# Kernel tuning notes

Measured on AMD Instinct MI355X. Metric: run time of the kernel, lower is better.

## Reference

```python
import jax, jax.numpy as jnp
import numpy as np

N_NODES = 100000
N_EDGES = 1600000
NUM_FEATURES = 128


def setup_inputs() -> dict:
    key = jax.random.key(0)
    ks = jax.random.split(key, 10)
    x = jax.random.normal(ks[0], (N_NODES, NUM_FEATURES), dtype=jnp.float32)
    edge_index = jax.random.randint(ks[1], (2, N_EDGES), 0, N_NODES, dtype=jnp.int64)
    # conv1 MLP: Linear(num_features,128) -> ReLU -> Linear(128,128)
    s1 = 1.0 / np.sqrt(NUM_FEATURES)
    W1 = jax.random.uniform(ks[2], (NUM_FEATURES, 128), jnp.float32, -s1, s1)
    b1 = jax.random.uniform(ks[3], (128,), jnp.float32, -s1, s1)
    s2 = 1.0 / np.sqrt(128)
    W2 = jax.random.uniform(ks[4], (128, 128), jnp.float32, -s2, s2)
    b2 = jax.random.uniform(ks[5], (128,), jnp.float32, -s2, s2)
    # conv2 MLP: Linear(128,64) -> ReLU -> Linear(64,64)
    W3 = jax.random.uniform(ks[6], (128, 64), jnp.float32, -s2, s2)
    b3 = jax.random.uniform(ks[7], (64,), jnp.float32, -s2, s2)
    s3 = 1.0 / np.sqrt(64)
    W4 = jax.random.uniform(ks[8], (64, 64), jnp.float32, -s3, s3)
    b4 = jax.random.uniform(ks[9], (64,), jnp.float32, -s3, s3)
    return {"x": x, "edge_index": edge_index, "W1": W1, "b1": b1,
            "W2": W2, "b2": b2, "W3": W3, "b3": b3, "W4": W4, "b4": b4}


def _gin_conv(x, src, dst, Wa, ba, Wb, bb):
    # GINConv with eps=0: out = MLP(x + sum_{j->i} x_j)
    agg = jax.ops.segment_sum(x[src], dst, num_segments=N_NODES)
    h = x + agg
    h = jax.nn.relu(h @ Wa + ba)
    return h @ Wb + bb


def reference(x, edge_index, W1, b1, W2, b2, W3, b3, W4, b4):
    src, dst = edge_index[0], edge_index[1]
    h = jax.nn.relu(_gin_conv(x, src, dst, W1, b1, W2, b2))
    h = jax.nn.relu(_gin_conv(h, src, dst, W3, b3, W4, b4))
    return h
```

## Files before the change

kernel.cpp:

```cpp
#include <hip/hip_runtime.h>
#include <hip/hip_bf16.h>

#define NODES 100000
#define EDGES 1600000
#define NBINS ((NODES + 127) >> 7)
#define BINCAP 2560
#define PB_BLOCKS 256
#define PB_CHUNK ((EDGES + PB_BLOCKS - 1) / PB_BLOCKS)
#define CAST_BLOCKS 12500
#define WPREP_BLOCKS 176

typedef __bf16 bf16x8 __attribute__((ext_vector_type(8)));
typedef float f32x4 __attribute__((ext_vector_type(4)));

__device__ __forceinline__ unsigned short f2b(float f) {
  __hip_bfloat16 h = __float2bfloat16(f);
  return __builtin_bit_cast(unsigned short, h);
}
__device__ __forceinline__ float b_lo(unsigned u) { return __uint_as_float(u << 16); }
__device__ __forceinline__ float b_hi(unsigned u) { return __uint_as_float(u & 0xffff0000u); }

__global__ __launch_bounds__(256) void prep_count(
    const float4* __restrict__ x4, ushort4* __restrict__ xh4,
    const float* __restrict__ W1, const float* __restrict__ W2,
    const float* __restrict__ W3, const float* __restrict__ W4,
    unsigned short* __restrict__ Wt1, unsigned short* __restrict__ Wt2,
    unsigned short* __restrict__ Wt3, unsigned short* __restrict__ Wt4,
    int* __restrict__ cnt) {
  const int b = blockIdx.x;
  if (b < CAST_BLOCKS) {
    int i = b * 256 + threadIdx.x;
    float4 v = x4[i];
    ushort4 o;
    o.x = f2b(v.x); o.y = f2b(v.y); o.z = f2b(v.z); o.w = f2b(v.w);
    xh4[i] = o;
    return;
  }
  if (b < CAST_BLOCKS + WPREP_BLOCKS) {
    int i = (b - CAST_BLOCKS) * 256 + threadIdx.x;
    if (i < 16384) {
      int n = i >> 7, k = i & 127;
      Wt1[i] = f2b(W1[k * 128 + n]);
    } else if (i < 32768) {
      int j = i - 16384; int n = j >> 7, k = j & 127;
      Wt2[j] = f2b(W2[k * 128 + n]);
    } else if (i < 40960) {
      int j = i - 32768; int n = j >> 7, k = j & 127;
      Wt3[j] = f2b(W3[k * 64 + n]);
    } else if (i < 45056) {
      int j = i - 40960; int n = j >> 6, k = j & 63;
      Wt4[j] = f2b(W4[k * 64 + n]);
    }
    return;
  }
  for (int i = threadIdx.x; i < NBINS; i += 256) cnt[i] = 0;
}

__global__ __launch_bounds__(256) void bin_scatter(const int* __restrict__ src,
                                                   const int* __restrict__ dst,
                                                   int* __restrict__ cnt,
                                                   unsigned* __restrict__ coarse) {
  __shared__ int base[NBINS];
  __shared__ int h[NBINS];
  const int beg = blockIdx.x * PB_CHUNK;
  const int end = min(beg + PB_CHUNK, EDGES);
  for (int i = threadIdx.x; i < NBINS; i += 256) h[i] = 0;
  __syncthreads();
  for (int e = beg + threadIdx.x; e < end; e += 256)
    atomicAdd(&h[dst[e] >> 7], 1);
  __syncthreads();
  for (int i = threadIdx.x; i < NBINS; i += 256) {
    int c = h[i];
    if (c > 0) base[i] = atomicAdd(&cnt[i], c);
    h[i] = 0;
  }
  __syncthreads();
  for (int e = beg + threadIdx.x; e < end; e += 256) {
    int d = dst[e];
    int b = d >> 7;
    int pos = base[b] + atomicAdd(&h[b], 1);
    coarse[(size_t)b * BINCAP + pos] = (unsigned)src[e] | ((unsigned)(d & 127) << 17);
  }
}

__global__ __launch_bounds__(256) void bin_fine(const unsigned* __restrict__ coarse,
                                                const int* __restrict__ cnt,
                                                int2* __restrict__ rowpairs,
                                                int* __restrict__ bucket) {
  __shared__ unsigned ent[BINCAP];
  __shared__ unsigned obuf[BINCAP];
  __shared__ int deg[128];
  __shared__ int pre[128];
  const int b = blockIdx.x;
  const int t = threadIdx.x;
  const int s0 = b * BINCAP;
  const int nE = cnt[b];
  const int binBase = b << 7;

  if (t < 128) deg[t] = 0;
  __syncthreads();
  for (int i = t; i < nE; i += 256) {
    unsigned e = coarse[s0 + i];
    ent[i] = e;
    atomicAdd(&deg[e >> 17], 1);
  }
  __syncthreads();
  int v = 0;
  if (t < 128) {
    v = deg[t];
    pre[t] = v;
  }
  __syncthreads();
  for (int off = 1; off < 128; off <<= 1) {
    int u = (t >= off && t < 128) ? pre[t - off] : 0;
    __syncthreads();
    if (t < 128) pre[t] += u;
    __syncthreads();
  }
  if (t < 128) {
    int inc = pre[t];
    int ex = inc - v;
    if (binBase + t < NODES) rowpairs[binBase + t] = make_int2(s0 + ex, s0 + inc);
    deg[t] = ex;
  }
  __syncthreads();
  for (int i = t; i < nE; i += 256) {
    unsigned e = ent[i];
    int pos = atomicAdd(&deg[e >> 17], 1);
    obuf[pos] = e & 0x1FFFFu;
  }
  __syncthreads();
  for (int i = t; i < nE; i += 256) bucket[s0 + i] = (int)obuf[i];
}

#define ACC8(r, m)                                                            \
  a[0] = fmaf(b_lo(r.x), m, a[0]); a[1] = fmaf(b_hi(r.x), m, a[1]);           \
  a[2] = fmaf(b_lo(r.y), m, a[2]); a[3] = fmaf(b_hi(r.y), m, a[3]);           \
  a[4] = fmaf(b_lo(r.z), m, a[4]); a[5] = fmaf(b_hi(r.z), m, a[5]);           \
  a[6] = fmaf(b_lo(r.w), m, a[6]); a[7] = fmaf(b_hi(r.w), m, a[7]);

template <int K, int N1, int N2, bool OUT_F32>
__global__ __launch_bounds__(256, 6) void gin_layer(
    const uint4* __restrict__ xq, const int2* __restrict__ rowpairs,
    const int* __restrict__ bucket,
    const unsigned short* __restrict__ Wa, const float* __restrict__ ba,
    const unsigned short* __restrict__ Wb, const float* __restrict__ bb,
    void* __restrict__ Cout, int M) {
  constexpr int LDA = K + 8;
  constexpr int NT1 = N1 / 16, KB1 = K / 32;
  constexpr int NT2 = N2 / 16, KB2 = N1 / 32;
  __shared__ unsigned short S[64 * LDA];

  const int tid = threadIdx.x;
  const int wave = tid >> 6;
  const int lane = tid & 63;
  const int g = lane >> 4;
  const int fl = lane & 15;
  const int rowBase = blockIdx.x * 64;

  for (int p = 0; p < 4; p++) {
    const int rloc = wave * 16 + p * 4 + g;
    const int n = rowBase + rloc;
    float a[8] = {0.f, 0.f, 0.f, 0.f, 0.f, 0.f, 0.f, 0.f};
    if (n < M) {
      uint4 v = xq[(size_t)n * 16 + fl];
      a[0] = b_lo(v.x); a[1] = b_hi(v.x);
      a[2] = b_lo(v.y); a[3] = b_hi(v.y);
      a[4] = b_lo(v.z); a[5] = b_hi(v.z);
      a[6] = b_lo(v.w); a[7] = b_hi(v.w);
      const int2 se = rowpairs[n];
      const int beg = se.x, end = se.y;
      for (int j = beg; j < end; j += 8) {
        int i1 = min(j + 1, end - 1), i2 = min(j + 2, end - 1),
            i3 = min(j + 3, end - 1), i4 = min(j + 4, end - 1),
            i5 = min(j + 5, end - 1), i6 = min(j + 6, end - 1),
            i7 = min(j + 7, end - 1);
        int s0 = bucket[j],  s1 = bucket[i1], s2 = bucket[i2], s3 = bucket[i3];
        int s4 = bucket[i4], s5 = bucket[i5], s6 = bucket[i6], s7 = bucket[i7];
        uint4 r0 = xq[(size_t)s0 * 16 + fl];
        uint4 r1 = xq[(size_t)s1 * 16 + fl];
        uint4 r2 = xq[(size_t)s2 * 16 + fl];
        uint4 r3 = xq[(size_t)s3 * 16 + fl];
        uint4 r4 = xq[(size_t)s4 * 16 + fl];
        uint4 r5 = xq[(size_t)s5 * 16 + fl];
        uint4 r6 = xq[(size_t)s6 * 16 + fl];
        uint4 r7 = xq[(size_t)s7 * 16 + fl];
        float m1 = (j + 1 < end) ? 1.f : 0.f;
        float m2 = (j + 2 < end) ? 1.f : 0.f;
        float m3 = (j + 3 < end) ? 1.f : 0.f;
        float m4 = (j + 4 < end) ? 1.f : 0.f;
        float m5 = (j + 5 < end) ? 1.f : 0.f;
        float m6 = (j + 6 < end) ? 1.f : 0.f;
        float m7 = (j + 7 < end) ? 1.f : 0.f;
        ACC8(r0, 1.f) ACC8(r1, m1) ACC8(r2, m2) ACC8(r3, m3)
        ACC8(r4, m4) ACC8(r5, m5) ACC8(r6, m6) ACC8(r7, m7)
      }
    }
    uint4 o;
    o.x = ((unsigned)f2b(a[1]) << 16) | f2b(a[0]);
    o.y = ((unsigned)f2b(a[3]) << 16) | f2b(a[2]);
    o.z = ((unsigned)f2b(a[5]) << 16) | f2b(a[4]);
    o.w = ((unsigned)f2b(a[7]) << 16) | f2b(a[6]);
    *(uint4*)&S[rloc * LDA + fl * 8] = o;
  }

  const int arow = wave * 16 + fl;

  f32x4 acc[NT1];
#pragma unroll
  for (int c = 0; c < NT1; c++) acc[c] = (f32x4){0.f, 0.f, 0.f, 0.f};
#pragma unroll
  for (int kb = 0; kb < KB1; kb++) {
    bf16x8 av = *(const bf16x8*)&S[arow * LDA + kb * 32 + g * 8];
#pragma unroll
    for (int c = 0; c < NT1; c++) {
      bf16x8 bv = *(const bf16x8*)&Wa[(size_t)(c * 16 + fl) * K + kb * 32 + g * 8];
      acc[c] = __builtin_amdgcn_mfma_f32_16x16x32_bf16(av, bv, acc[c], 0, 0, 0);
    }
  }

#pragma unroll
  for (int c = 0; c < NT1; c++) {
    int col = c * 16 + fl;
    float bv = ba[col];
#pragma unroll
    for (int reg = 0; reg < 4; reg++) {
      int rloc = wave * 16 + g * 4 + reg;
      S[rloc * LDA + col] = f2b(fmaxf(acc[c][reg] + bv, 0.f));
    }
  }

  f32x4 acc2[NT2];
#pragma unroll
  for (int c = 0; c < NT2; c++) acc2[c] = (f32x4){0.f, 0.f, 0.f, 0.f};
#pragma unroll
  for (int kb = 0; kb < KB2; kb++) {
    bf16x8 av = *(const bf16x8*)&S[arow * LDA + kb * 32 + g * 8];
#pragma unroll
    for (int c = 0; c < NT2; c++) {
      bf16x8 bv = *(const bf16x8*)&Wb[(size_t)(c * 16 + fl) * N1 + kb * 32 + g * 8];
      acc2[c] = __builtin_amdgcn_mfma_f32_16x16x32_bf16(av, bv, acc2[c], 0, 0, 0);
    }
  }

#pragma unroll
  for (int c = 0; c < NT2; c++) {
    int col = c * 16 + fl;
    float bv = bb[col];
#pragma unroll
    for (int reg = 0; reg < 4; reg++) {
      int row = rowBase + wave * 16 + g * 4 + reg;
      if (row < M) {
        float v = fmaxf(acc2[c][reg] + bv, 0.f);
        if (OUT_F32)
          ((float*)Cout)[(size_t)row * N2 + col] = v;
        else
          ((unsigned short*)Cout)[(size_t)row * N2 + col] = f2b(v);
      }
    }
  }
}

extern "C" void kernel_launch(void* const* d_in, const int* in_sizes, int n_in,
                              void* d_out, int out_size, void* d_ws, size_t ws_size,
                              hipStream_t stream) {
  const float* x = (const float*)d_in[0];
  const int* ei = (const int*)d_in[1];
  const int* src = ei;
  const int* dst = ei + EDGES;
  const float* W1 = (const float*)d_in[2];
  const float* b1 = (const float*)d_in[3];
  const float* W2 = (const float*)d_in[4];
  const float* b2 = (const float*)d_in[5];
  const float* W3 = (const float*)d_in[6];
  const float* b3 = (const float*)d_in[7];
  const float* W4 = (const float*)d_in[8];
  const float* b4 = (const float*)d_in[9];
  float* out = (float*)d_out;

  char* ws = (char*)d_ws;
  unsigned short* xh = (unsigned short*)ws;
  unsigned short* hB = xh + (size_t)NODES * 128;
  unsigned short* Wt1 = hB + (size_t)NODES * 128;
  unsigned short* Wt2 = Wt1 + 128 * 128;
  unsigned short* Wt3 = Wt2 + 128 * 128;
  unsigned short* Wt4 = Wt3 + 64 * 128;
  int2* rowpairs = (int2*)(Wt4 + 64 * 64);
  int* cnt = (int*)(rowpairs + NODES);
  unsigned* coarse = (unsigned*)(cnt + 784);
  int* bucket = (int*)(coarse + (size_t)NBINS * BINCAP);

  const int gblocks = (NODES + 63) / 64;

  prep_count<<<CAST_BLOCKS + WPREP_BLOCKS + 1, 256, 0, stream>>>(
      (const float4*)x, (ushort4*)xh, W1, W2, W3, W4, Wt1, Wt2, Wt3, Wt4, cnt);
  bin_scatter<<<PB_BLOCKS, 256, 0, stream>>>(src, dst, cnt, coarse);
  bin_fine<<<NBINS, 256, 0, stream>>>(coarse, cnt, rowpairs, bucket);

  gin_layer<128, 128, 128, false><<<gblocks, 256, 0, stream>>>(
      (const uint4*)xh, rowpairs, bucket, Wt1, b1, Wt2, b2, hB, NODES);
  gin_layer<128, 64, 64, true><<<gblocks, 256, 0, stream>>>(
      (const uint4*)hB, rowpairs, bucket, Wt3, b3, Wt4, b4, out, NODES);
}
```

Baseline: 369.7 us.

## Stage MLP weight tiles in shared memory for MFMA B operands

The fused GIN layer kernel now copies 64-row slices of each weight matrix into a padded LDS buffer and reads the MFMA B operands from LDS instead of global memory. The per-block global weight traffic becomes a cooperative coalesced load that is shared across the four waves. In exchange it adds block-wide barriers between slices, a second LDS array, and a lower occupancy hint in launch bounds (6 to 4 blocks per CU). The extra barriers may also expose the latency of the irregular gather phase.

```diff
diff --git a/kernel.cpp b/kernel.cpp
--- a/kernel.cpp
+++ b/kernel.cpp
@@ -140,16 +140,21 @@
   a[6] = fmaf(b_lo(r.w), m, a[6]); a[7] = fmaf(b_hi(r.w), m, a[7]);
 
 template <int K, int N1, int N2, bool OUT_F32>
-__global__ __launch_bounds__(256, 6) void gin_layer(
+__global__ __launch_bounds__(256, 4) void gin_layer(
     const uint4* __restrict__ xq, const int2* __restrict__ rowpairs,
     const int* __restrict__ bucket,
     const unsigned short* __restrict__ Wa, const float* __restrict__ ba,
     const unsigned short* __restrict__ Wb, const float* __restrict__ bb,
     void* __restrict__ Cout, int M) {
   constexpr int LDA = K + 8;
+  constexpr int LWA = K + 8;
+  constexpr int LWB = N1 + 8;
   constexpr int NT1 = N1 / 16, KB1 = K / 32;
   constexpr int NT2 = N2 / 16, KB2 = N1 / 32;
+  constexpr int NH1 = N1 / 64;
+  constexpr int NH2 = N2 / 64;
   __shared__ unsigned short S[64 * LDA];
+  __shared__ unsigned short Wl[64 * LWA];
 
   const int tid = threadIdx.x;
   const int wave = tid >> 6;
@@ -157,6 +162,11 @@
   const int g = lane >> 4;
   const int fl = lane & 15;
   const int rowBase = blockIdx.x * 64;
+
+  for (int i = tid; i < 64 * (K / 8); i += 256) {
+    int n = i / (K / 8), c2 = i % (K / 8);
+    *(uint4*)&Wl[n * LWA + c2 * 8] = *(const uint4*)&Wa[(size_t)n * K + c2 * 8];
+  }
 
   for (int p = 0; p < 4; p++) {
     const int rloc = wave * 16 + p * 4 + g;
@@ -203,6 +213,7 @@
     o.w = ((unsigned)f2b(a[7]) << 16) | f2b(a[6]);
     *(uint4*)&S[rloc * LDA + fl * 8] = o;
   }
+  __syncthreads();
 
   const int arow = wave * 16 + fl;
 
@@ -210,12 +221,25 @@
 #pragma unroll
   for (int c = 0; c < NT1; c++) acc[c] = (f32x4){0.f, 0.f, 0.f, 0.f};
 #pragma unroll
-  for (int kb = 0; kb < KB1; kb++) {
-    bf16x8 av = *(const bf16x8*)&S[arow * LDA + kb * 32 + g * 8];
-#pragma unroll
-    for (int c = 0; c < NT1; c++) {
-      bf16x8 bv = *(const bf16x8*)&Wa[(size_t)(c * 16 + fl) * K + kb * 32 + g * 8];
-      acc[c] = __builtin_amdgcn_mfma_f32_16x16x32_bf16(av, bv, acc[c], 0, 0, 0);
+  for (int h = 0; h < NH1; h++) {
+    if (h > 0) {
+      __syncthreads();
+      for (int i = tid; i < 64 * (K / 8); i += 256) {
+        int n = i / (K / 8), c2 = i % (K / 8);
+        *(uint4*)&Wl[n * LWA + c2 * 8] =
+            *(const uint4*)&Wa[(size_t)(h * 64 + n) * K + c2 * 8];
+      }
+      __syncthreads();
+    }
+#pragma unroll
+    for (int kb = 0; kb < KB1; kb++) {
+      bf16x8 av = *(const bf16x8*)&S[arow * LDA + kb * 32 + g * 8];
+#pragma unroll
+      for (int cl = 0; cl < 4; cl++) {
+        bf16x8 bv = *(const bf16x8*)&Wl[(cl * 16 + fl) * LWA + kb * 32 + g * 8];
+        acc[h * 4 + cl] =
+            __builtin_amdgcn_mfma_f32_16x16x32_bf16(av, bv, acc[h * 4 + cl], 0, 0, 0);
+      }
     }
   }
 
@@ -234,12 +258,23 @@
 #pragma unroll
   for (int c = 0; c < NT2; c++) acc2[c] = (f32x4){0.f, 0.f, 0.f, 0.f};
 #pragma unroll
-  for (int kb = 0; kb < KB2; kb++) {
-    bf16x8 av = *(const bf16x8*)&S[arow * LDA + kb * 32 + g * 8];
-#pragma unroll
-    for (int c = 0; c < NT2; c++) {
-      bf16x8 bv = *(const bf16x8*)&Wb[(size_t)(c * 16 + fl) * N1 + kb * 32 + g * 8];
-      acc2[c] = __builtin_amdgcn_mfma_f32_16x16x32_bf16(av, bv, acc2[c], 0, 0, 0);
+  for (int h = 0; h < NH2; h++) {
+    __syncthreads();
+    for (int i = tid; i < 64 * (N1 / 8); i += 256) {
+      int n = i / (N1 / 8), c2 = i % (N1 / 8);
+      *(uint4*)&Wl[n * LWB + c2 * 8] =
+          *(const uint4*)&Wb[(size_t)(h * 64 + n) * N1 + c2 * 8];
+    }
+    __syncthreads();
+#pragma unroll
+    for (int kb = 0; kb < KB2; kb++) {
+      bf16x8 av = *(const bf16x8*)&S[arow * LDA + kb * 32 + g * 8];
+#pragma unroll
+      for (int cl = 0; cl < 4; cl++) {
+        bf16x8 bv = *(const bf16x8*)&Wl[(cl * 16 + fl) * LWB + kb * 32 + g * 8];
+        acc2[h * 4 + cl] =
+            __builtin_amdgcn_mfma_f32_16x16x32_bf16(av, bv, acc2[h * 4 + cl], 0, 0, 0);
+      }
     }
   }
 
```

After: 311.6 us, median of 2. 15.7% less time.
